# Performance work log

Hardware: AMD Instinct MI355X
Metric: run time of the kernel (lower is better)

The kernel has to match this reference:

```python
import jax, jax.numpy as jnp
import numpy as np

N_ATOMS = 200_000
AVG_NEIGHBORS = 64
N_PAIRS = N_ATOMS * AVG_NEIGHBORS
BOX = 60.0  # Angstrom, so cutoff=10 masks most random pairs (realistic neighbor-list sparsity)


def setup_inputs() -> dict:
    key = jax.random.key(0)
    kR, ki, kj = jax.random.split(key, 3)
    R = jax.random.uniform(kR, (N_ATOMS, 3), dtype=jnp.float32) * BOX
    idx_i = jax.random.randint(ki, (N_PAIRS,), 0, N_ATOMS, dtype=jnp.int32)
    idx_j = jax.random.randint(kj, (N_PAIRS,), 0, N_ATOMS, dtype=jnp.int32)
    # learned scalar parameters from __init__
    epsilon = jnp.float32(0.238)
    sigma = jnp.float32(3.4)
    cutoff = jnp.float32(10.0)
    return {"R": R, "epsilon": epsilon, "sigma": sigma, "cutoff": cutoff,
            "idx_i": idx_i, "idx_j": idx_j}


def reference(R, epsilon, sigma, cutoff, idx_i, idx_j):
    """LJ 12-6 pairwise potential over a neighbor list.

    Returns (energy [N] per-atom, forces [N,3]).
    Each (i,j) pair appears in both directions in the pair list, hence the 0.5
    factor on per-atom energy; forces accumulate per direction (action-reaction
    handled by the symmetric pair list).
    """
    n_atoms = R.shape[0]
    rij = R[idx_i] - R[idx_j]                     # [P,3] gather
    r2 = jnp.sum(rij * rij, axis=-1)              # [P]
    mask = (r2 < cutoff * cutoff) & (r2 > 1e-10)  # inside cutoff, exclude coincident
    r2s = jnp.where(mask, r2, 1.0)                # safe divide
    sr2 = (sigma * sigma) / r2s
    sr6 = sr2 * sr2 * sr2
    sr12 = sr6 * sr6
    e_pair = jnp.where(mask, 4.0 * epsilon * (sr12 - sr6), 0.0)          # [P]
    f_mag = jnp.where(mask, 24.0 * epsilon * (2.0 * sr12 - sr6) / r2s, 0.0)
    f_pair = f_mag[:, None] * rij                 # [P,3]
    energy = 0.5 * jax.ops.segment_sum(e_pair, idx_i, num_segments=n_atoms)   # [N]
    forces = jax.ops.segment_sum(f_pair, idx_i, num_segments=n_atoms)         # [N,3]
    return energy, forces
```

## Files before the change

kernel.cpp:

```cpp
#include <hip/hip_runtime.h>


typedef int   v4i __attribute__((ext_vector_type(4)));
typedef float v4f __attribute__((ext_vector_type(4)));

#define CELL_SZ   15.0f
#define INV_CELL  (1.0f / 15.0f)
#define GRP       8
#define WGT       1024
#define NWG       1024

__global__ void __launch_bounds__(256) pad_R_kernel(
    const float* __restrict__ R, v4f* __restrict__ Rp, int n_atoms)
{
    int a = blockIdx.x * blockDim.x + threadIdx.x;
    if (a < n_atoms) {
        v4f v;
        v.x = R[3 * a + 0];
        v.y = R[3 * a + 1];
        v.z = R[3 * a + 2];
        v.w = 0.0f;
        Rp[a] = v;
    }
}

__global__ void __launch_bounds__(256) cell_kernel(
    const float* __restrict__ R, unsigned* __restrict__ packed, int n_atoms)
{
    int t = blockIdx.x * blockDim.x + threadIdx.x;
    int n_thr = (n_atoms + 15) >> 4;
    if (t >= n_thr) return;
    int a0 = t << 4;
    unsigned w[3] = {0u, 0u, 0u};
#pragma unroll
    for (int k = 0; k < 16; ++k) {
        int a = a0 + k;
        unsigned c = 0u;
        if (a < n_atoms) {
            int cx = min(3, max(0, (int)(R[3 * a + 0] * INV_CELL)));
            int cy = min(3, max(0, (int)(R[3 * a + 1] * INV_CELL)));
            int cz = min(3, max(0, (int)(R[3 * a + 2] * INV_CELL)));
            c = (unsigned)(cx | (cy << 2) | (cz << 4));
        }
        int bit = 6 * k, word = bit >> 5, off = bit & 31;
        w[word] |= c << off;
        if (off > 26) w[word + 1] |= c >> (32 - off);
    }
    packed[3 * t + 0] = w[0];
    packed[3 * t + 1] = w[1];
    packed[3 * t + 2] = w[2];
}

__device__ __forceinline__ unsigned cell6(const unsigned char* c8, unsigned a) {
    unsigned bit = a * 6u;
    unsigned by  = bit >> 3;
    unsigned v   = (unsigned)c8[by] | ((unsigned)c8[by + 1] << 8);
    return (v >> (bit & 7u)) & 63u;
}

__global__ void __launch_bounds__(WGT) lj_filter_kernel(
    const v4f* __restrict__ Rp,
    const unsigned* __restrict__ packed,
    const int* __restrict__ idx_i,
    const int* __restrict__ idx_j,
    const float* __restrict__ eps_p,
    const float* __restrict__ sig_p,
    const float* __restrict__ cut_p,
    float* __restrict__ energy,
    float* __restrict__ forces,
    int n_pairs, int pk_words, int chunk)
{
    extern __shared__ unsigned lds[];
    for (int w = threadIdx.x; w < pk_words; w += WGT)
        lds[w] = packed[w];
    __syncthreads();
    const unsigned char* c8 = (const unsigned char*)lds;

    const float eps  = eps_p[0];
    const float sig  = sig_p[0];
    const float cut  = cut_p[0];
    const float s2   = sig * sig;
    const float cut2 = cut * cut;
    const bool nofilter = (cut2 > CELL_SZ * CELL_SZ);

    const int cs = blockIdx.x * chunk;
    const int ce = min(cs + chunk, n_pairs);

    for (int p = cs + threadIdx.x * GRP; p < ce; p += WGT * GRP) {
        int is8[GRP], js8[GRP];
        if (p + GRP <= n_pairs) {
            v4i a0 = __builtin_nontemporal_load((const v4i*)idx_i + (p >> 2));
            v4i a1 = __builtin_nontemporal_load((const v4i*)idx_i + (p >> 2) + 1);
            v4i b0 = __builtin_nontemporal_load((const v4i*)idx_j + (p >> 2));
            v4i b1 = __builtin_nontemporal_load((const v4i*)idx_j + (p >> 2) + 1);
            is8[0] = a0.x; is8[1] = a0.y; is8[2] = a0.z; is8[3] = a0.w;
            is8[4] = a1.x; is8[5] = a1.y; is8[6] = a1.z; is8[7] = a1.w;
            js8[0] = b0.x; js8[1] = b0.y; js8[2] = b0.z; js8[3] = b0.w;
            js8[4] = b1.x; js8[5] = b1.y; js8[6] = b1.z; js8[7] = b1.w;
        } else {
            for (int k = 0; k < GRP; ++k) {
                is8[k] = (p + k < n_pairs) ? idx_i[p + k] : 0;
                js8[k] = (p + k < n_pairs) ? idx_j[p + k] : 0;
            }
        }

        unsigned m = 0u;
#pragma unroll
        for (int k = 0; k < GRP; ++k) {
            unsigned ci = cell6(c8, (unsigned)is8[k]);
            unsigned cj = cell6(c8, (unsigned)js8[k]);
            int ddx = (int)(ci & 3u)        - (int)(cj & 3u);
            int ddy = (int)((ci >> 2) & 3u) - (int)((cj >> 2) & 3u);
            int ddz = (int)(ci >> 4)        - (int)(cj >> 4);
            bool ok = ((unsigned)(ddx + 1) <= 2u) & ((unsigned)(ddy + 1) <= 2u)
                    & ((unsigned)(ddz + 1) <= 2u);
            if (ok | nofilter) m |= (1u << k);
        }

        v4f Ri[GRP], Rj[GRP];
#pragma unroll
        for (int k = 0; k < GRP; ++k)
            if (m & (1u << k)) { Ri[k] = Rp[is8[k]]; Rj[k] = Rp[js8[k]]; }

#pragma unroll
        for (int k = 0; k < GRP; ++k) {
            if (m & (1u << k)) {
                const float dx = Ri[k].x - Rj[k].x;
                const float dy = Ri[k].y - Rj[k].y;
                const float dz = Ri[k].z - Rj[k].z;
                const float r2 = dx * dx + dy * dy + dz * dz;
                if (r2 < cut2 && r2 > 1e-10f) {
                    const float inv  = 1.0f / r2;
                    const float sr2  = s2 * inv;
                    const float sr6  = sr2 * sr2 * sr2;
                    const float sr12 = sr6 * sr6;
                    const float e    = 2.0f * eps * (sr12 - sr6);
                    const float f    = 24.0f * eps * (2.0f * sr12 - sr6) * inv;
                    const int i = is8[k];
                    atomicAdd(&energy[i], e);
                    atomicAdd(&forces[3 * i + 0], f * dx);
                    atomicAdd(&forces[3 * i + 1], f * dy);
                    atomicAdd(&forces[3 * i + 2], f * dz);
                }
            }
        }
    }
}

#define PPT 8
__global__ void __launch_bounds__(256) lj_pairs_fb_kernel(
    const v4f* __restrict__ Rp,
    const v4i* __restrict__ idx_i4, const v4i* __restrict__ idx_j4,
    const float* __restrict__ eps_p, const float* __restrict__ sig_p,
    const float* __restrict__ cut_p,
    float* __restrict__ energy, float* __restrict__ forces, int n_oct)
{
    int t = blockIdx.x * blockDim.x + threadIdx.x;
    if (t >= n_oct) return;
    const float eps  = eps_p[0];
    const float sig  = sig_p[0];
    const float cut  = cut_p[0];
    const float s2   = sig * sig;
    const float cut2 = cut * cut;
    v4i ii0 = __builtin_nontemporal_load(idx_i4 + 2 * t);
    v4i ii1 = __builtin_nontemporal_load(idx_i4 + 2 * t + 1);
    v4i jj0 = __builtin_nontemporal_load(idx_j4 + 2 * t);
    v4i jj1 = __builtin_nontemporal_load(idx_j4 + 2 * t + 1);
    int is[PPT] = { ii0.x, ii0.y, ii0.z, ii0.w, ii1.x, ii1.y, ii1.z, ii1.w };
    int js[PPT] = { jj0.x, jj0.y, jj0.z, jj0.w, jj1.x, jj1.y, jj1.z, jj1.w };
    v4f Ri[PPT], Rj[PPT];
#pragma unroll
    for (int k = 0; k < PPT; ++k) Ri[k] = Rp[is[k]];
#pragma unroll
    for (int k = 0; k < PPT; ++k) Rj[k] = Rp[js[k]];
#pragma unroll
    for (int k = 0; k < PPT; ++k) {
        const float dx = Ri[k].x - Rj[k].x;
        const float dy = Ri[k].y - Rj[k].y;
        const float dz = Ri[k].z - Rj[k].z;
        const float r2 = dx * dx + dy * dy + dz * dz;
        if (r2 < cut2 && r2 > 1e-10f) {
            const float inv  = 1.0f / r2;
            const float sr2  = s2 * inv;
            const float sr6  = sr2 * sr2 * sr2;
            const float sr12 = sr6 * sr6;
            const float e    = 2.0f * eps * (sr12 - sr6);
            const float f    = 24.0f * eps * (2.0f * sr12 - sr6) * inv;
            const int i = is[k];
            atomicAdd(&energy[i], e);
            atomicAdd(&forces[3 * i + 0], f * dx);
            atomicAdd(&forces[3 * i + 1], f * dy);
            atomicAdd(&forces[3 * i + 2], f * dz);
        }
    }
}

__global__ void lj_pairs_fb_tail_kernel(
    const v4f* __restrict__ Rp,
    const int* __restrict__ idx_i, const int* __restrict__ idx_j,
    const float* __restrict__ eps_p, const float* __restrict__ sig_p,
    const float* __restrict__ cut_p,
    float* __restrict__ energy, float* __restrict__ forces,
    int start, int n_pairs)
{
    int p = start + blockIdx.x * blockDim.x + threadIdx.x;
    if (p >= n_pairs) return;
    const float eps  = eps_p[0];
    const float sig  = sig_p[0];
    const float cut  = cut_p[0];
    const float s2   = sig * sig;
    const float cut2 = cut * cut;
    const int i = idx_i[p];
    v4f A = Rp[i];
    v4f B = Rp[idx_j[p]];
    const float dx = A.x - B.x, dy = A.y - B.y, dz = A.z - B.z;
    const float r2 = dx * dx + dy * dy + dz * dz;
    if (r2 < cut2 && r2 > 1e-10f) {
        const float inv  = 1.0f / r2;
        const float sr2  = s2 * inv;
        const float sr6  = sr2 * sr2 * sr2;
        const float sr12 = sr6 * sr6;
        const float e    = 2.0f * eps * (sr12 - sr6);
        const float f    = 24.0f * eps * (2.0f * sr12 - sr6) * inv;
        atomicAdd(&energy[i], e);
        atomicAdd(&forces[3 * i + 0], f * dx);
        atomicAdd(&forces[3 * i + 1], f * dy);
        atomicAdd(&forces[3 * i + 2], f * dz);
    }
}

extern "C" void kernel_launch(void* const* d_in, const int* in_sizes, int n_in,
                              void* d_out, int out_size, void* d_ws, size_t ws_size,
                              hipStream_t stream) {
    const float* R     = (const float*)d_in[0];
    const float* eps_p = (const float*)d_in[1];
    const float* sig_p = (const float*)d_in[2];
    const float* cut_p = (const float*)d_in[3];
    const int*   idx_i = (const int*)d_in[4];
    const int*   idx_j = (const int*)d_in[5];

    const int n_atoms = in_sizes[0] / 3;
    const int n_pairs = in_sizes[4];

    float* energy = (float*)d_out;
    float* forces = (float*)d_out + n_atoms;

    hipMemsetAsync(d_out, 0, (size_t)out_size * sizeof(float), stream);

    char* ws = (char*)d_ws;
    const size_t rp_b     = (((size_t)n_atoms * 16) + 255) & ~(size_t)255;
    const int    n_thr    = (n_atoms + 15) >> 4;
    const int    pk_store = 3 * n_thr;
    const int    pk_words = pk_store + 1;
    const size_t pk_b     = (((size_t)pk_words * 4) + 255) & ~(size_t)255;
    const size_t lds_b    = (((size_t)pk_words * 4) + 15) & ~(size_t)15;

    const bool have_rp    = ws_size >= rp_b;
    const bool use_filter = have_rp && (ws_size >= rp_b + pk_b)
                            && (lds_b <= 160000);

    v4f*      Rp     = (v4f*)ws;
    unsigned* packed = (unsigned*)(ws + rp_b);

    if (have_rp) {
        int blocks = (n_atoms + 255) / 256;
        pad_R_kernel<<<blocks, 256, 0, stream>>>(R, Rp, n_atoms);
    }

    if (use_filter) {
        int cblocks = (n_thr + 255) / 256;
        cell_kernel<<<cblocks, 256, 0, stream>>>(R, packed, n_atoms);

        hipFuncSetAttribute((const void*)lj_filter_kernel,
                            hipFuncAttributeMaxDynamicSharedMemorySize,
                            (int)lds_b);

        int chunk = (((n_pairs + NWG - 1) / NWG) + GRP - 1) & ~(GRP - 1);
        lj_filter_kernel<<<NWG, WGT, lds_b, stream>>>(
            Rp, packed, idx_i, idx_j, eps_p, sig_p, cut_p,
            energy, forces, n_pairs, pk_words, chunk);
    } else {
        const int n_oct = n_pairs / PPT;
        const int start = n_oct * PPT;
        if (n_oct > 0) {
            int blocks = (n_oct + 255) / 256;
            lj_pairs_fb_kernel<<<blocks, 256, 0, stream>>>(
                Rp, (const v4i*)idx_i, (const v4i*)idx_j,
                eps_p, sig_p, cut_p, energy, forces, n_oct);
        }
        if (start < n_pairs) {
            lj_pairs_fb_tail_kernel<<<1, 64, 0, stream>>>(
                Rp, idx_i, idx_j, eps_p, sig_p, cut_p,
                energy, forces, start, n_pairs);
        }
    }
}
```

Baseline: 210.2 us.

## Use cutoff-sized 2D cell filter and fewer persistent filter workgroups

The cell prefilter now bins atoms into an x/y grid whose cell size equals the runtime cutoff, up to 8 cells per axis, instead of fixed 15 Å 3D cells. Only pairs in adjacent x/y cells fetch coordinates, which rejects more far pairs before the random gathers. The filter kernel also launches 256 workgroups instead of 1024, so the packed cell table is copied into LDS far fewer times, at the cost of coarser load balancing. The LJ math is factored into a shared helper without changing its behaviour.

```diff
diff --git a/kernel.cpp b/kernel.cpp
--- a/kernel.cpp
+++ b/kernel.cpp
@@ -4,11 +4,9 @@
 typedef int   v4i __attribute__((ext_vector_type(4)));
 typedef float v4f __attribute__((ext_vector_type(4)));
 
-#define CELL_SZ   15.0f
-#define INV_CELL  (1.0f / 15.0f)
-#define GRP       8
-#define WGT       1024
-#define NWG       1024
+#define GRP    8
+#define WGT    1024
+#define NWG_F  256
 
 __global__ void __launch_bounds__(256) pad_R_kernel(
     const float* __restrict__ R, v4f* __restrict__ Rp, int n_atoms)
@@ -25,11 +23,13 @@
 }
 
 __global__ void __launch_bounds__(256) cell_kernel(
-    const float* __restrict__ R, unsigned* __restrict__ packed, int n_atoms)
+    const float* __restrict__ R, const float* __restrict__ cut_p,
+    unsigned* __restrict__ packed, int n_atoms)
 {
     int t = blockIdx.x * blockDim.x + threadIdx.x;
     int n_thr = (n_atoms + 15) >> 4;
     if (t >= n_thr) return;
+    const float inv_cut = 1.0f / cut_p[0];
     int a0 = t << 4;
     unsigned w[3] = {0u, 0u, 0u};
 #pragma unroll
@@ -37,10 +37,9 @@
         int a = a0 + k;
         unsigned c = 0u;
         if (a < n_atoms) {
-            int cx = min(3, max(0, (int)(R[3 * a + 0] * INV_CELL)));
-            int cy = min(3, max(0, (int)(R[3 * a + 1] * INV_CELL)));
-            int cz = min(3, max(0, (int)(R[3 * a + 2] * INV_CELL)));
-            c = (unsigned)(cx | (cy << 2) | (cz << 4));
+            int cx = min(7, max(0, (int)(R[3 * a + 0] * inv_cut)));
+            int cy = min(7, max(0, (int)(R[3 * a + 1] * inv_cut)));
+            c = (unsigned)(cx | (cy << 3));
         }
         int bit = 6 * k, word = bit >> 5, off = bit & 31;
         w[word] |= c << off;
@@ -58,7 +57,27 @@
     return (v >> (bit & 7u)) & 63u;
 }
 
-__global__ void __launch_bounds__(WGT) lj_filter_kernel(
+__device__ __forceinline__ void lj_body(
+    v4f A, v4f B, float eps, float s2, float cut2, int gi,
+    float* __restrict__ energy, float* __restrict__ forces)
+{
+    const float dx = A.x - B.x, dy = A.y - B.y, dz = A.z - B.z;
+    const float r2 = dx * dx + dy * dy + dz * dz;
+    if (r2 < cut2 && r2 > 1e-10f) {
+        const float inv  = 1.0f / r2;
+        const float sr2  = s2 * inv;
+        const float sr6  = sr2 * sr2 * sr2;
+        const float sr12 = sr6 * sr6;
+        const float e    = 2.0f * eps * (sr12 - sr6);
+        const float f    = 24.0f * eps * (2.0f * sr12 - sr6) * inv;
+        atomicAdd(&energy[gi], e);
+        atomicAdd(&forces[3 * gi + 0], f * dx);
+        atomicAdd(&forces[3 * gi + 1], f * dy);
+        atomicAdd(&forces[3 * gi + 2], f * dz);
+    }
+}
+
+__global__ void __launch_bounds__(WGT) lj_fused_kernel(
     const v4f* __restrict__ Rp,
     const unsigned* __restrict__ packed,
     const int* __restrict__ idx_i,
@@ -81,7 +100,6 @@
     const float cut  = cut_p[0];
     const float s2   = sig * sig;
     const float cut2 = cut * cut;
-    const bool nofilter = (cut2 > CELL_SZ * CELL_SZ);
 
     const int cs = blockIdx.x * chunk;
     const int ce = min(cs + chunk, n_pairs);
@@ -98,9 +116,11 @@
             js8[0] = b0.x; js8[1] = b0.y; js8[2] = b0.z; js8[3] = b0.w;
             js8[4] = b1.x; js8[5] = b1.y; js8[6] = b1.z; js8[7] = b1.w;
         } else {
+#pragma unroll
             for (int k = 0; k < GRP; ++k) {
-                is8[k] = (p + k < n_pairs) ? idx_i[p + k] : 0;
-                js8[k] = (p + k < n_pairs) ? idx_j[p + k] : 0;
+                bool v = (p + k < n_pairs);
+                is8[k] = v ? idx_i[p + k] : 0;
+                js8[k] = v ? idx_j[p + k] : 0;
             }
         }
 
@@ -109,12 +129,10 @@
         for (int k = 0; k < GRP; ++k) {
             unsigned ci = cell6(c8, (unsigned)is8[k]);
             unsigned cj = cell6(c8, (unsigned)js8[k]);
-            int ddx = (int)(ci & 3u)        - (int)(cj & 3u);
-            int ddy = (int)((ci >> 2) & 3u) - (int)((cj >> 2) & 3u);
-            int ddz = (int)(ci >> 4)        - (int)(cj >> 4);
-            bool ok = ((unsigned)(ddx + 1) <= 2u) & ((unsigned)(ddy + 1) <= 2u)
-                    & ((unsigned)(ddz + 1) <= 2u);
-            if (ok | nofilter) m |= (1u << k);
+            int ddx = (int)(ci & 7u) - (int)(cj & 7u);
+            int ddy = (int)(ci >> 3) - (int)(cj >> 3);
+            bool ok = ((unsigned)(ddx + 1) <= 2u) & ((unsigned)(ddy + 1) <= 2u);
+            if (ok) m |= (1u << k);
         }
 
         v4f Ri[GRP], Rj[GRP];
@@ -123,27 +141,9 @@
             if (m & (1u << k)) { Ri[k] = Rp[is8[k]]; Rj[k] = Rp[js8[k]]; }
 
 #pragma unroll
-        for (int k = 0; k < GRP; ++k) {
-            if (m & (1u << k)) {
-                const float dx = Ri[k].x - Rj[k].x;
-                const float dy = Ri[k].y - Rj[k].y;
-                const float dz = Ri[k].z - Rj[k].z;
-                const float r2 = dx * dx + dy * dy + dz * dz;
-                if (r2 < cut2 && r2 > 1e-10f) {
-                    const float inv  = 1.0f / r2;
-                    const float sr2  = s2 * inv;
-                    const float sr6  = sr2 * sr2 * sr2;
-                    const float sr12 = sr6 * sr6;
-                    const float e    = 2.0f * eps * (sr12 - sr6);
-                    const float f    = 24.0f * eps * (2.0f * sr12 - sr6) * inv;
-                    const int i = is8[k];
-                    atomicAdd(&energy[i], e);
-                    atomicAdd(&forces[3 * i + 0], f * dx);
-                    atomicAdd(&forces[3 * i + 1], f * dy);
-                    atomicAdd(&forces[3 * i + 2], f * dz);
-                }
-            }
-        }
+        for (int k = 0; k < GRP; ++k)
+            if (m & (1u << k))
+                lj_body(Ri[k], Rj[k], eps, s2, cut2, is8[k], energy, forces);
     }
 }
 
@@ -174,25 +174,8 @@
 #pragma unroll
     for (int k = 0; k < PPT; ++k) Rj[k] = Rp[js[k]];
 #pragma unroll
-    for (int k = 0; k < PPT; ++k) {
-        const float dx = Ri[k].x - Rj[k].x;
-        const float dy = Ri[k].y - Rj[k].y;
-        const float dz = Ri[k].z - Rj[k].z;
-        const float r2 = dx * dx + dy * dy + dz * dz;
-        if (r2 < cut2 && r2 > 1e-10f) {
-            const float inv  = 1.0f / r2;
-            const float sr2  = s2 * inv;
-            const float sr6  = sr2 * sr2 * sr2;
-            const float sr12 = sr6 * sr6;
-            const float e    = 2.0f * eps * (sr12 - sr6);
-            const float f    = 24.0f * eps * (2.0f * sr12 - sr6) * inv;
-            const int i = is[k];
-            atomicAdd(&energy[i], e);
-            atomicAdd(&forces[3 * i + 0], f * dx);
-            atomicAdd(&forces[3 * i + 1], f * dy);
-            atomicAdd(&forces[3 * i + 2], f * dz);
-        }
-    }
+    for (int k = 0; k < PPT; ++k)
+        lj_body(Ri[k], Rj[k], eps, s2, cut2, is[k], energy, forces);
 }
 
 __global__ void lj_pairs_fb_tail_kernel(
@@ -205,28 +188,11 @@
 {
     int p = start + blockIdx.x * blockDim.x + threadIdx.x;
     if (p >= n_pairs) return;
-    const float eps  = eps_p[0];
-    const float sig  = sig_p[0];
-    const float cut  = cut_p[0];
-    const float s2   = sig * sig;
-    const float cut2 = cut * cut;
-    const int i = idx_i[p];
-    v4f A = Rp[i];
-    v4f B = Rp[idx_j[p]];
-    const float dx = A.x - B.x, dy = A.y - B.y, dz = A.z - B.z;
-    const float r2 = dx * dx + dy * dy + dz * dz;
-    if (r2 < cut2 && r2 > 1e-10f) {
-        const float inv  = 1.0f / r2;
-        const float sr2  = s2 * inv;
-        const float sr6  = sr2 * sr2 * sr2;
-        const float sr12 = sr6 * sr6;
-        const float e    = 2.0f * eps * (sr12 - sr6);
-        const float f    = 24.0f * eps * (2.0f * sr12 - sr6) * inv;
-        atomicAdd(&energy[i], e);
-        atomicAdd(&forces[3 * i + 0], f * dx);
-        atomicAdd(&forces[3 * i + 1], f * dy);
-        atomicAdd(&forces[3 * i + 2], f * dz);
-    }
+    const float eps = eps_p[0];
+    const float sig = sig_p[0];
+    const float cut = cut_p[0];
+    lj_body(Rp[idx_i[p]], Rp[idx_j[p]], eps, sig * sig, cut * cut,
+            idx_i[p], energy, forces);
 }
 
 extern "C" void kernel_launch(void* const* d_in, const int* in_sizes, int n_in,
@@ -245,13 +211,12 @@
     float* energy = (float*)d_out;
     float* forces = (float*)d_out + n_atoms;
 
-    hipMemsetAsync(d_out, 0, (size_t)out_size * sizeof(float), stream);
+    (void)hipMemsetAsync(d_out, 0, (size_t)out_size * sizeof(float), stream);
 
     char* ws = (char*)d_ws;
     const size_t rp_b     = (((size_t)n_atoms * 16) + 255) & ~(size_t)255;
     const int    n_thr    = (n_atoms + 15) >> 4;
-    const int    pk_store = 3 * n_thr;
-    const int    pk_words = pk_store + 1;
+    const int    pk_words = 3 * n_thr + 1;
     const size_t pk_b     = (((size_t)pk_words * 4) + 255) & ~(size_t)255;
     const size_t lds_b    = (((size_t)pk_words * 4) + 15) & ~(size_t)15;
 
@@ -269,14 +234,14 @@
 
     if (use_filter) {
         int cblocks = (n_thr + 255) / 256;
-        cell_kernel<<<cblocks, 256, 0, stream>>>(R, packed, n_atoms);
-
-        hipFuncSetAttribute((const void*)lj_filter_kernel,
-                            hipFuncAttributeMaxDynamicSharedMemorySize,
-                            (int)lds_b);
-
-        int chunk = (((n_pairs + NWG - 1) / NWG) + GRP - 1) & ~(GRP - 1);
-        lj_filter_kernel<<<NWG, WGT, lds_b, stream>>>(
+        cell_kernel<<<cblocks, 256, 0, stream>>>(R, cut_p, packed, n_atoms);
+
+        (void)hipFuncSetAttribute((const void*)lj_fused_kernel,
+                                  hipFuncAttributeMaxDynamicSharedMemorySize,
+                                  (int)lds_b);
+
+        int chunk = (((n_pairs + NWG_F - 1) / NWG_F) + GRP - 1) & ~(GRP - 1);
+        lj_fused_kernel<<<NWG_F, WGT, lds_b, stream>>>(
             Rp, packed, idx_i, idx_j, eps_p, sig_p, cut_p,
             energy, forces, n_pairs, pk_words, chunk);
     } else {
```

Result: faster. 192.6 us (-8.4%).
